# Kernel tuning notes

Measured on AMD Instinct MI355X. Metric: run time of the kernel, lower is better.

Reference implementation:

```python
import jax, jax.numpy as jnp
import numpy as np

N = 50000   # nodes
E = 800000  # edges (avg degree 16)
D = 96      # in = hid = out
BN_EPS = 1e-5


def setup_inputs() -> dict:
    key = jax.random.key(0)
    ks = jax.random.split(key, 16)
    features = jax.random.normal(ks[0], (N, D), jnp.float32)
    src = jax.random.randint(ks[1], (E,), 0, N)
    dst = jax.random.randint(ks[2], (E,), 0, N)
    bound = 1.0 / np.sqrt(D)
    def lin(kw, kb):
        W = jax.random.uniform(kw, (D, D), jnp.float32, -bound, bound)
        b = jax.random.uniform(kb, (D,), jnp.float32, -bound, bound)
        return W, b
    W1, b1 = lin(ks[3], ks[4])
    W2, b2 = lin(ks[5], ks[6])
    W3, b3 = lin(ks[7], ks[8])
    gamma1 = jnp.ones((D,), jnp.float32)
    beta1 = jnp.zeros((D,), jnp.float32)
    gamma2 = jnp.ones((D,), jnp.float32)
    beta2 = jnp.zeros((D,), jnp.float32)
    return dict(features=features, W1=W1, b1=b1, gamma1=gamma1, beta1=beta1,
                W2=W2, b2=b2, gamma2=gamma2, beta2=beta2, W3=W3, b3=b3,
                src=src, dst=dst)


def _gin_conv(h, W, b, src, dst, inv_deg):
    # mean-aggregate incoming neighbor features, eps = 0: (h + mean_nb) @ W + b
    agg = jax.ops.segment_sum(h[src], dst, num_segments=N) * inv_deg[:, None]
    return (h + agg) @ W + b


def _batchnorm(x, gamma, beta):
    mu = jnp.mean(x, axis=0)
    var = jnp.mean((x - mu) ** 2, axis=0)  # biased, as torch BN training
    return (x - mu) * jax.lax.rsqrt(var + BN_EPS) * gamma + beta


def reference(features, W1, b1, gamma1, beta1, W2, b2, gamma2, beta2, W3, b3, src, dst):
    deg = jax.ops.segment_sum(jnp.ones((E,), jnp.float32), dst, num_segments=N)
    inv_deg = jnp.where(deg > 0, 1.0 / jnp.maximum(deg, 1.0), 0.0)
    h = _gin_conv(features, W1, b1, src, dst, inv_deg)
    h = jax.nn.relu(_batchnorm(h, gamma1, beta1))  # dropout p=0 -> identity
    h = _gin_conv(h, W2, b2, src, dst, inv_deg)
    h = jax.nn.relu(_batchnorm(h, gamma2, beta2))
    h = _gin_conv(h, W3, b3, src, dst, inv_deg)
    return h
```

## Files before the change

### kernel.cpp

```cpp
#include <hip/hip_runtime.h>

#define FD 96
#define BSH 7
#define BNODES 128
#define NBLK 256

typedef float  f32x4 __attribute__((ext_vector_type(4)));
typedef short  s16x8 __attribute__((ext_vector_type(8)));

__device__ __forceinline__ unsigned short f2bf(float x) {
    unsigned u = __float_as_uint(x);
    u = (u + 0x7fffu + ((u >> 16) & 1u)) >> 16;
    return (unsigned short)u;
}
__device__ __forceinline__ float bflo(unsigned u) { return __uint_as_float(u << 16); }
__device__ __forceinline__ float bfhi(unsigned u) { return __uint_as_float(u & 0xffff0000u); }

__device__ __forceinline__ s16x8 pack8(const float t[8]) {
    union { unsigned u[4]; s16x8 v; } r;
    #pragma unroll
    for (int z = 0; z < 4; z++)
        r.u[z] = (unsigned)f2bf(t[2 * z]) | ((unsigned)f2bf(t[2 * z + 1]) << 16);
    return r.v;
}

#define ACC8(R, T) { \
    T[0] += bflo(R.x); T[1] += bfhi(R.x); \
    T[2] += bflo(R.y); T[3] += bfhi(R.y); \
    T[4] += bflo(R.z); T[5] += bfhi(R.z); \
    T[6] += bflo(R.w); T[7] += bfhi(R.w); }

#define FIN8(R, T, id) { \
    T[0] = fmaf(id, T[0], bflo(R.x)); T[1] = fmaf(id, T[1], bfhi(R.x)); \
    T[2] = fmaf(id, T[2], bflo(R.y)); T[3] = fmaf(id, T[3], bfhi(R.y)); \
    T[4] = fmaf(id, T[4], bflo(R.z)); T[5] = fmaf(id, T[5], bfhi(R.z)); \
    T[6] = fmaf(id, T[6], bflo(R.w)); T[7] = fmaf(id, T[7], bfhi(R.w)); }


__global__ void k_h2d(const int* __restrict__ dst, int* __restrict__ hist2d,
                      int* __restrict__ bcnt, int E, int nbkt, int chunk) {
    __shared__ int hist[512];
    int tid = threadIdx.x, b = blockIdx.x;
    for (int i = tid; i < 512; i += 256) hist[i] = 0;
    __syncthreads();
    int lo = b * chunk, hi = min(lo + chunk, E);
    for (int i = lo + tid; i < hi; i += 256)
        atomicAdd(&hist[dst[i] >> BSH], 1);
    __syncthreads();
    for (int q = tid; q < nbkt; q += 256) {
        int hv = hist[q];
        hist2d[(size_t)q * NBLK + b] = hv;
        if (hv) atomicAdd(&bcnt[q], hv);
    }
}

__global__ void k_bscan(const int* __restrict__ bcnt, int* __restrict__ bbase, int nbkt) {
    __shared__ int sh[512];
    int tid = threadIdx.x;
    int v = (tid < nbkt) ? bcnt[tid] : 0;
    sh[tid] = v;
    __syncthreads();
    for (int off = 1; off < 512; off <<= 1) {
        int t = (tid >= off) ? sh[tid - off] : 0;
        __syncthreads();
        sh[tid] += t;
        __syncthreads();
    }
    int incl = sh[tid];
    if (tid < nbkt) bbase[tid] = incl - v;
    if (tid == nbkt - 1) bbase[nbkt] = incl;
}

__global__ void k_cscan(const int* __restrict__ hist2d, const int* __restrict__ bbase,
                        int* __restrict__ cursor2d) {
    __shared__ int sh[NBLK];
    int q = blockIdx.x, tid = threadIdx.x;
    int v = hist2d[(size_t)q * NBLK + tid];
    sh[tid] = v;
    __syncthreads();
    for (int off = 1; off < NBLK; off <<= 1) {
        int t = (tid >= off) ? sh[tid - off] : 0;
        __syncthreads();
        sh[tid] += t;
        __syncthreads();
    }
    cursor2d[(size_t)q * NBLK + tid] = bbase[q] + sh[tid] - v;
}

__global__ void k_scat(const int* __restrict__ src, const int* __restrict__ dst,
                       const int* __restrict__ cursor2d, uint2* __restrict__ ebuf,
                       int E, int nbkt, int chunk) {
    __shared__ int cur[512];
    int tid = threadIdx.x, b = blockIdx.x;
    for (int q = tid; q < nbkt; q += 256)
        cur[q] = cursor2d[(size_t)q * NBLK + b];
    __syncthreads();
    int lo = b * chunk, hi = min(lo + chunk, E);
    for (int i = lo + tid; i < hi; i += 256) {
        int d = dst[i];
        int p = atomicAdd(&cur[d >> BSH], 1);
        ebuf[p] = make_uint2((unsigned)d, (unsigned)src[i]);
    }
}

__global__ void k_bsort(const uint2* __restrict__ ebuf, const int* __restrict__ bbase,
                        int* __restrict__ csr, int* __restrict__ rp2, int* __restrict__ re2,
                        float* __restrict__ invd2, int* __restrict__ perm,
                        int* __restrict__ inv_perm, int n) {
    __shared__ int cnt[BNODES];
    __shared__ int cur[BNODES];
    __shared__ int dh[64];
    const int b = blockIdx.x;
    const int tid = threadIdx.x;
    const int lo = bbase[b], hi = bbase[b + 1];
    if (tid < BNODES) cnt[tid] = 0;
    if (tid < 64) dh[tid] = 0;
    __syncthreads();
    for (int i = lo + tid; i < hi; i += blockDim.x)
        atomicAdd(&cnt[(int)ebuf[i].x - (b << BSH)], 1);
    __syncthreads();
    const int node = (b << BSH) + tid;
    const int v = (tid < BNODES) ? cnt[tid] : 0;
    const int dcl = min(v, 63);
    if (tid < BNODES && node < n) atomicAdd(&dh[dcl], 1);
    for (int off = 1; off < BNODES; off <<= 1) {
        int t = (tid < BNODES && tid >= off) ? cnt[tid - off] : 0;
        __syncthreads();
        if (tid < BNODES) cnt[tid] += t;
        __syncthreads();
    }
    int dv = (tid < 64) ? dh[tid] : 0;
    for (int off = 1; off < 64; off <<= 1) {
        int t = (tid < 64 && tid >= off) ? dh[tid - off] : 0;
        __syncthreads();
        if (tid < 64) dh[tid] += t;
        __syncthreads();
    }
    if (tid < 64) dh[tid] -= dv;
    __syncthreads();
    if (tid < BNODES) {
        int excl = cnt[tid] - v;
        if (node < n) {
            int rk = atomicAdd(&dh[dcl], 1);
            int slot = (b << BSH) + rk;
            perm[slot] = node;
            inv_perm[node] = slot;
            rp2[slot] = lo + excl;
            re2[slot] = lo + excl + v;
            invd2[slot] = (v > 0) ? (1.0f / (float)v) : 0.f;
        }
        cur[tid] = excl;
    }
    __syncthreads();
    for (int i = lo + tid; i < hi; i += blockDim.x) {
        uint2 e2 = ebuf[i];
        int local = (int)e2.x - (b << BSH);
        int p = lo + atomicAdd(&cur[local], 1);
        csr[p] = (int)e2.y;
    }
}

__global__ void k_xlate(int* __restrict__ csr, const int* __restrict__ inv_perm, int E) {
    int i = blockIdx.x * blockDim.x + threadIdx.x;
    if (i < E) csr[i] = inv_perm[csr[i]];
}

__global__ void k_cvtp(const float* __restrict__ feat, const int* __restrict__ perm,
                       uint4* __restrict__ o, int n) {
    int g = blockIdx.x * blockDim.x + threadIdx.x;
    int i = g / 12;
    if (i >= n) return;
    int q = g - i * 12;
    int node = perm[i];
    const float4* row = (const float4*)(feat + (size_t)node * FD);
    float4 x = row[2 * q], y = row[2 * q + 1];
    uint4 r;
    r.x = (unsigned)f2bf(x.x) | ((unsigned)f2bf(x.y) << 16);
    r.y = (unsigned)f2bf(x.z) | ((unsigned)f2bf(x.w) << 16);
    r.z = (unsigned)f2bf(y.x) | ((unsigned)f2bf(y.y) << 16);
    r.w = (unsigned)f2bf(y.z) | ((unsigned)f2bf(y.w) << 16);
    o[g] = r;
}

__global__ void k_wprep3(const float* __restrict__ W1, const float* __restrict__ W2,
                         const float* __restrict__ W3, unsigned short* __restrict__ Wt) {
    int i = blockIdx.x * blockDim.x + threadIdx.x;
    if (i >= 3 * FD * FD) return;
    int m = i / (FD * FD), r = i - m * FD * FD;
    const float* W = (m == 0) ? W1 : ((m == 1) ? W2 : W3);
    int col = r % FD, k = r / FD;
    Wt[m * FD * FD + col * FD + k] = f2bf(W[r]);
}


template<int STATS, int OBF>
__global__ __launch_bounds__(256) void k_fused(
    const uint4* __restrict__ h,
    const int* __restrict__ rp2, const int* __restrict__ re2,
    const float* __restrict__ invd2, const int* __restrict__ csr2,
    const int* __restrict__ perm,
    const unsigned short* __restrict__ Wt, const float* __restrict__ bias,
    unsigned short* __restrict__ yb, float* __restrict__ yf,
    float* __restrict__ accg, int n)
{
    __shared__ float sred[2 * FD];
    const int tid = threadIdx.x, lane = tid & 63;
    const int r16 = lane & 15, hg = lane >> 4;
    const int tbase = blockIdx.x * 64 + (tid >> 6) * 16;
    const int idx = tbase + r16;

    float t0[8], t1[8], t2[8];
    #pragma unroll
    for (int z = 0; z < 8; z++) { t0[z] = 0.f; t1[z] = 0.f; t2[z] = 0.f; }

    if (idx < n) {
        int e = rp2[idx];
        const int end = re2[idx];
        for (; e + 4 <= end; e += 4) {
            int ca = csr2[e], cb = csr2[e + 1], cc = csr2[e + 2], cd = csr2[e + 3];
            uint4 A0 = h[(size_t)ca * 12 + hg], A1 = h[(size_t)ca * 12 + 4 + hg], A2 = h[(size_t)ca * 12 + 8 + hg];
            uint4 B0 = h[(size_t)cb * 12 + hg], B1 = h[(size_t)cb * 12 + 4 + hg], B2 = h[(size_t)cb * 12 + 8 + hg];
            uint4 C0 = h[(size_t)cc * 12 + hg], C1 = h[(size_t)cc * 12 + 4 + hg], C2 = h[(size_t)cc * 12 + 8 + hg];
            uint4 D0 = h[(size_t)cd * 12 + hg], D1 = h[(size_t)cd * 12 + 4 + hg], D2 = h[(size_t)cd * 12 + 8 + hg];
            ACC8(A0, t0); ACC8(A1, t1); ACC8(A2, t2);
            ACC8(B0, t0); ACC8(B1, t1); ACC8(B2, t2);
            ACC8(C0, t0); ACC8(C1, t1); ACC8(C2, t2);
            ACC8(D0, t0); ACC8(D1, t1); ACC8(D2, t2);
        }
        for (; e < end; e++) {
            int c = csr2[e];
            uint4 R0 = h[(size_t)c * 12 + hg], R1 = h[(size_t)c * 12 + 4 + hg], R2 = h[(size_t)c * 12 + 8 + hg];
            ACC8(R0, t0); ACC8(R1, t1); ACC8(R2, t2);
        }
        const float id = invd2[idx];
        uint4 S0 = h[(size_t)idx * 12 + hg], S1 = h[(size_t)idx * 12 + 4 + hg], S2 = h[(size_t)idx * 12 + 8 + hg];
        FIN8(S0, t0, id); FIN8(S1, t1, id); FIN8(S2, t2, id);
    }

    s16x8 a0 = pack8(t0), a1 = pack8(t1), a2 = pack8(t2);

    f32x4 acc[6];
    #pragma unroll
    for (int c2 = 0; c2 < 6; c2++) acc[c2] = (f32x4){0.f, 0.f, 0.f, 0.f};
    #pragma unroll
    for (int c2 = 0; c2 < 6; c2++) {
        const unsigned short* wp = Wt + (size_t)(c2 * 16 + r16) * FD + hg * 8;
        s16x8 b0 = *(const s16x8*)(wp);
        s16x8 b1 = *(const s16x8*)(wp + 32);
        s16x8 b2 = *(const s16x8*)(wp + 64);
        acc[c2] = __builtin_amdgcn_mfma_f32_16x16x32_bf16(a0, b0, acc[c2], 0, 0, 0);
        acc[c2] = __builtin_amdgcn_mfma_f32_16x16x32_bf16(a1, b1, acc[c2], 0, 0, 0);
        acc[c2] = __builtin_amdgcn_mfma_f32_16x16x32_bf16(a2, b2, acc[c2], 0, 0, 0);
    }

    int orow[4];
    #pragma unroll
    for (int j = 0; j < 4; j++) {
        int rr = tbase + hg * 4 + j;
        orow[j] = (!OBF && rr < n) ? perm[rr] : rr;
    }
    float s1v[6], s2v[6];
    #pragma unroll
    for (int c2 = 0; c2 < 6; c2++) { s1v[c2] = 0.f; s2v[c2] = 0.f; }
    #pragma unroll
    for (int c2 = 0; c2 < 6; c2++) {
        float bc = bias[c2 * 16 + r16];
        #pragma unroll
        for (int j = 0; j < 4; j++) {
            int rr = tbase + hg * 4 + j;
            if (rr < n) {
                float y = acc[c2][j] + bc;
                if (OBF) yb[(size_t)rr * FD + c2 * 16 + r16] = f2bf(y);
                else     yf[(size_t)orow[j] * FD + c2 * 16 + r16] = y;
                if (STATS) { s1v[c2] += y; s2v[c2] = fmaf(y, y, s2v[c2]); }
            }
        }
    }
    if (STATS) {
        if (tid < 2 * FD) sred[tid] = 0.f;
        __syncthreads();
        #pragma unroll
        for (int c2 = 0; c2 < 6; c2++) {
            float v1 = s1v[c2], v2 = s2v[c2];
            v1 += __shfl_xor(v1, 16, 64); v1 += __shfl_xor(v1, 32, 64);
            v2 += __shfl_xor(v2, 16, 64); v2 += __shfl_xor(v2, 32, 64);
            if (lane < 16) {
                atomicAdd(&sred[c2 * 16 + r16], v1);
                atomicAdd(&sred[FD + c2 * 16 + r16], v2);
            }
        }
        __syncthreads();
        if (tid < 2 * FD) atomicAdd(&accg[tid], sred[tid]);
    }
}

__global__ void k_bnfin(const float* __restrict__ acc,
                        const float* __restrict__ gamma, const float* __restrict__ beta,
                        float* __restrict__ na, float* __restrict__ nc, float invN) {
    int f = threadIdx.x;
    float mu  = acc[f] * invN;
    float var = acc[FD + f] * invN - mu * mu;
    float a = gamma[f] * rsqrtf(var + 1e-5f);
    na[f] = a;
    nc[f] = beta[f] - mu * a;
}

__global__ void k_norm(uint4* __restrict__ y, const float* __restrict__ na,
                       const float* __restrict__ nc, int n12) {
    int g = blockIdx.x * blockDim.x + threadIdx.x;
    if (g >= n12) return;
    int q = g % 12;
    float4 a0 = *(const float4*)(na + q * 8), a1 = *(const float4*)(na + q * 8 + 4);
    float4 c0 = *(const float4*)(nc + q * 8), c1 = *(const float4*)(nc + q * 8 + 4);
    uint4 r = y[g];
    float v0 = fmaxf(fmaf(a0.x, bflo(r.x), c0.x), 0.f);
    float v1 = fmaxf(fmaf(a0.y, bfhi(r.x), c0.y), 0.f);
    float v2 = fmaxf(fmaf(a0.z, bflo(r.y), c0.z), 0.f);
    float v3 = fmaxf(fmaf(a0.w, bfhi(r.y), c0.w), 0.f);
    float v4 = fmaxf(fmaf(a1.x, bflo(r.z), c1.x), 0.f);
    float v5 = fmaxf(fmaf(a1.y, bfhi(r.z), c1.y), 0.f);
    float v6 = fmaxf(fmaf(a1.z, bflo(r.w), c1.z), 0.f);
    float v7 = fmaxf(fmaf(a1.w, bfhi(r.w), c1.w), 0.f);
    uint4 pk;
    pk.x = (unsigned)f2bf(v0) | ((unsigned)f2bf(v1) << 16);
    pk.y = (unsigned)f2bf(v2) | ((unsigned)f2bf(v3) << 16);
    pk.z = (unsigned)f2bf(v4) | ((unsigned)f2bf(v5) << 16);
    pk.w = (unsigned)f2bf(v6) | ((unsigned)f2bf(v7) << 16);
    y[g] = pk;
}

extern "C" void kernel_launch(void* const* d_in, const int* in_sizes, int n_in,
                              void* d_out, int out_size, void* d_ws, size_t ws_size,
                              hipStream_t stream) {
    const float* feat = (const float*)d_in[0];
    const float* W1   = (const float*)d_in[1];
    const float* b1   = (const float*)d_in[2];
    const float* g1   = (const float*)d_in[3];
    const float* be1  = (const float*)d_in[4];
    const float* W2   = (const float*)d_in[5];
    const float* b2   = (const float*)d_in[6];
    const float* g2   = (const float*)d_in[7];
    const float* be2  = (const float*)d_in[8];
    const float* W3   = (const float*)d_in[9];
    const float* b3   = (const float*)d_in[10];
    const int*   src  = (const int*)d_in[11];
    const int*   dst  = (const int*)d_in[12];

    const int n = in_sizes[0] / FD;
    const int e = in_sizes[11];
    const int nbkt = (n + BNODES - 1) >> BSH;
    const int chunk = (e + NBLK - 1) / NBLK;

    char* w = (char*)d_ws;
    unsigned short* hA  = (unsigned short*)w; w += (size_t)n * FD * 2;
    unsigned short* hB  = (unsigned short*)w; w += (size_t)n * FD * 2;
    unsigned short* Wt  = (unsigned short*)w; w += (size_t)3 * FD * FD * 2;
    int*   csr     = (int*)w;   w += (size_t)e * 4;
    int*   bcnt    = (int*)w;   w += 512 * 4;
    float* acc1    = (float*)w; w += 2 * FD * 4;
    float* acc2    = (float*)w; w += 2 * FD * 4;
    int*   bbase   = (int*)w;   w += 513 * 4;
    int*   hist2d  = (int*)w;   w += (size_t)512 * NBLK * 4;
    int*   cursor2d= (int*)w;   w += (size_t)512 * NBLK * 4;
    int*   rp2     = (int*)w;   w += (size_t)n * 4;
    int*   re2     = (int*)w;   w += (size_t)n * 4;
    float* invd2   = (float*)w; w += (size_t)n * 4;
    int*   perm    = (int*)w;   w += (size_t)n * 4;
    int*   invp    = (int*)w;   w += (size_t)n * 4;
    float* na1     = (float*)w; w += FD * 4;
    float* nc1     = (float*)w; w += FD * 4;
    float* na2     = (float*)w; w += FD * 4;
    float* nc2     = (float*)w; w += FD * 4;

    uint2* ebuf = (uint2*)hB;

    float* O = (float*)d_out;
    const float invN = 1.0f / (float)n;
    const int FUSE_GRID = (n + 63) / 64;
    const int n12 = n * 12;

    hipMemsetAsync(bcnt, 0, (512 + 4 * FD) * 4, stream);
    k_h2d<<<NBLK, 256, 0, stream>>>(dst, hist2d, bcnt, e, nbkt, chunk);
    k_bscan<<<1, 512, 0, stream>>>(bcnt, bbase, nbkt);
    k_cscan<<<nbkt, NBLK, 0, stream>>>(hist2d, bbase, cursor2d);
    k_scat<<<NBLK, 256, 0, stream>>>(src, dst, cursor2d, ebuf, e, nbkt, chunk);
    k_bsort<<<nbkt, 256, 0, stream>>>(ebuf, bbase, csr, rp2, re2, invd2, perm, invp, n);
    k_xlate<<<(e + 255) / 256, 256, 0, stream>>>(csr, invp, e);
    k_cvtp<<<(n12 + 255) / 256, 256, 0, stream>>>(feat, perm, (uint4*)hA, n);
    k_wprep3<<<(3 * FD * FD + 255) / 256, 256, 0, stream>>>(W1, W2, W3, Wt);

    k_fused<1, 1><<<FUSE_GRID, 256, 0, stream>>>((const uint4*)hA, rp2, re2, invd2, csr,
                                                 perm, Wt, b1, hB, nullptr, acc1, n);
    k_bnfin<<<1, FD, 0, stream>>>(acc1, g1, be1, na1, nc1, invN);
    k_norm<<<(n12 + 255) / 256, 256, 0, stream>>>((uint4*)hB, na1, nc1, n12);

    k_fused<1, 1><<<FUSE_GRID, 256, 0, stream>>>((const uint4*)hB, rp2, re2, invd2, csr,
                                                 perm, Wt + FD * FD, b2, hA, nullptr, acc2, n);
    k_bnfin<<<1, FD, 0, stream>>>(acc2, g2, be2, na2, nc2, invN);
    k_norm<<<(n12 + 255) / 256, 256, 0, stream>>>((uint4*)hA, na2, nc2, n12);

    k_fused<0, 0><<<FUSE_GRID, 256, 0, stream>>>((const uint4*)hA, rp2, re2, invd2, csr,
                                                 perm, Wt + 2 * FD * FD, b3, nullptr, O, nullptr, n);
}
```

Before: 237.0 us.

## Split each node's edge list across two waves and reduce partial sums in LDS

```diff
diff --git a/kernel.cpp b/kernel.cpp
--- a/kernel.cpp
+++ b/kernel.cpp
@@ -203,10 +203,15 @@
     unsigned short* __restrict__ yb, float* __restrict__ yf,
     float* __restrict__ accg, int n)
 {
+    __shared__ float part[2][24][64];
     __shared__ float sred[2 * FD];
-    const int tid = threadIdx.x, lane = tid & 63;
+    const int tid = threadIdx.x;
+    const int lane = tid & 63;
+    const int wv = tid >> 6;
+    const int tile = wv & 1;
+    const int low = (wv < 2);
     const int r16 = lane & 15, hg = lane >> 4;
-    const int tbase = blockIdx.x * 64 + (tid >> 6) * 16;
+    const int tbase = blockIdx.x * 32 + tile * 16;
     const int idx = tbase + r16;
 
     float t0[8], t1[8], t2[8];
@@ -214,9 +219,12 @@
     for (int z = 0; z < 8; z++) { t0[z] = 0.f; t1[z] = 0.f; t2[z] = 0.f; }
 
     if (idx < n) {
-        int e = rp2[idx];
+        const int beg = rp2[idx];
         const int end = re2[idx];
-        for (; e + 4 <= end; e += 4) {
+        const int mid = beg + ((end - beg) >> 1);
+        int e        = low ? beg : mid;
+        const int e2 = low ? mid : end;
+        for (; e + 4 <= e2; e += 4) {
             int ca = csr2[e], cb = csr2[e + 1], cc = csr2[e + 2], cd = csr2[e + 3];
             uint4 A0 = h[(size_t)ca * 12 + hg], A1 = h[(size_t)ca * 12 + 4 + hg], A2 = h[(size_t)ca * 12 + 8 + hg];
             uint4 B0 = h[(size_t)cb * 12 + hg], B1 = h[(size_t)cb * 12 + 4 + hg], B2 = h[(size_t)cb * 12 + 8 + hg];
@@ -227,55 +235,78 @@
             ACC8(C0, t0); ACC8(C1, t1); ACC8(C2, t2);
             ACC8(D0, t0); ACC8(D1, t1); ACC8(D2, t2);
         }
-        for (; e < end; e++) {
+        for (; e < e2; e++) {
             int c = csr2[e];
             uint4 R0 = h[(size_t)c * 12 + hg], R1 = h[(size_t)c * 12 + 4 + hg], R2 = h[(size_t)c * 12 + 8 + hg];
             ACC8(R0, t0); ACC8(R1, t1); ACC8(R2, t2);
         }
-        const float id = invd2[idx];
-        uint4 S0 = h[(size_t)idx * 12 + hg], S1 = h[(size_t)idx * 12 + 4 + hg], S2 = h[(size_t)idx * 12 + 8 + hg];
-        FIN8(S0, t0, id); FIN8(S1, t1, id); FIN8(S2, t2, id);
-    }
-
-    s16x8 a0 = pack8(t0), a1 = pack8(t1), a2 = pack8(t2);
-
-    f32x4 acc[6];
-    #pragma unroll
-    for (int c2 = 0; c2 < 6; c2++) acc[c2] = (f32x4){0.f, 0.f, 0.f, 0.f};
-    #pragma unroll
-    for (int c2 = 0; c2 < 6; c2++) {
-        const unsigned short* wp = Wt + (size_t)(c2 * 16 + r16) * FD + hg * 8;
-        s16x8 b0 = *(const s16x8*)(wp);
-        s16x8 b1 = *(const s16x8*)(wp + 32);
-        s16x8 b2 = *(const s16x8*)(wp + 64);
-        acc[c2] = __builtin_amdgcn_mfma_f32_16x16x32_bf16(a0, b0, acc[c2], 0, 0, 0);
-        acc[c2] = __builtin_amdgcn_mfma_f32_16x16x32_bf16(a1, b1, acc[c2], 0, 0, 0);
-        acc[c2] = __builtin_amdgcn_mfma_f32_16x16x32_bf16(a2, b2, acc[c2], 0, 0, 0);
-    }
-
-    int orow[4];
-    #pragma unroll
-    for (int j = 0; j < 4; j++) {
-        int rr = tbase + hg * 4 + j;
-        orow[j] = (!OBF && rr < n) ? perm[rr] : rr;
-    }
+    }
+
+    if (!low) {
+        #pragma unroll
+        for (int z = 0; z < 8; z++) {
+            part[tile][z][lane]      = t0[z];
+            part[tile][8 + z][lane]  = t1[z];
+            part[tile][16 + z][lane] = t2[z];
+        }
+    }
+    __syncthreads();
+
     float s1v[6], s2v[6];
     #pragma unroll
     for (int c2 = 0; c2 < 6; c2++) { s1v[c2] = 0.f; s2v[c2] = 0.f; }
-    #pragma unroll
-    for (int c2 = 0; c2 < 6; c2++) {
-        float bc = bias[c2 * 16 + r16];
+
+    if (low) {
+        #pragma unroll
+        for (int z = 0; z < 8; z++) {
+            t0[z] += part[tile][z][lane];
+            t1[z] += part[tile][8 + z][lane];
+            t2[z] += part[tile][16 + z][lane];
+        }
+        if (idx < n) {
+            const float id = invd2[idx];
+            uint4 S0 = h[(size_t)idx * 12 + hg], S1 = h[(size_t)idx * 12 + 4 + hg], S2 = h[(size_t)idx * 12 + 8 + hg];
+            FIN8(S0, t0, id); FIN8(S1, t1, id); FIN8(S2, t2, id);
+        }
+
+        s16x8 a0 = pack8(t0), a1 = pack8(t1), a2 = pack8(t2);
+
+        f32x4 acc[6];
+        #pragma unroll
+        for (int c2 = 0; c2 < 6; c2++) acc[c2] = (f32x4){0.f, 0.f, 0.f, 0.f};
+        #pragma unroll
+        for (int c2 = 0; c2 < 6; c2++) {
+            const unsigned short* wp = Wt + (size_t)(c2 * 16 + r16) * FD + hg * 8;
+            s16x8 b0 = *(const s16x8*)(wp);
+            s16x8 b1 = *(const s16x8*)(wp + 32);
+            s16x8 b2 = *(const s16x8*)(wp + 64);
+            acc[c2] = __builtin_amdgcn_mfma_f32_16x16x32_bf16(a0, b0, acc[c2], 0, 0, 0);
+            acc[c2] = __builtin_amdgcn_mfma_f32_16x16x32_bf16(a1, b1, acc[c2], 0, 0, 0);
+            acc[c2] = __builtin_amdgcn_mfma_f32_16x16x32_bf16(a2, b2, acc[c2], 0, 0, 0);
+        }
+
+        int orow[4];
         #pragma unroll
         for (int j = 0; j < 4; j++) {
             int rr = tbase + hg * 4 + j;
-            if (rr < n) {
-                float y = acc[c2][j] + bc;
-                if (OBF) yb[(size_t)rr * FD + c2 * 16 + r16] = f2bf(y);
-                else     yf[(size_t)orow[j] * FD + c2 * 16 + r16] = y;
-                if (STATS) { s1v[c2] += y; s2v[c2] = fmaf(y, y, s2v[c2]); }
+            orow[j] = (!OBF && rr < n) ? perm[rr] : rr;
+        }
+        #pragma unroll
+        for (int c2 = 0; c2 < 6; c2++) {
+            float bc = bias[c2 * 16 + r16];
+            #pragma unroll
+            for (int j = 0; j < 4; j++) {
+                int rr = tbase + hg * 4 + j;
+                if (rr < n) {
+                    float y = acc[c2][j] + bc;
+                    if (OBF) yb[(size_t)rr * FD + c2 * 16 + r16] = f2bf(y);
+                    else     yf[(size_t)orow[j] * FD + c2 * 16 + r16] = y;
+                    if (STATS) { s1v[c2] += y; s2v[c2] = fmaf(y, y, s2v[c2]); }
+                }
             }
         }
     }
+
     if (STATS) {
         if (tid < 2 * FD) sred[tid] = 0.f;
         __syncthreads();
@@ -376,7 +407,7 @@
 
     float* O = (float*)d_out;
     const float invN = 1.0f / (float)n;
-    const int FUSE_GRID = (n + 63) / 64;
+    const int FUSE_GRID = (n + 31) / 32;
     const int n12 = n * 12;
 
     hipMemsetAsync(bcnt, 0, (512 + 4 * FD) * 4, stream);
```

Measured after the change: 265.4 us. 12.0% more time.
